# Kernel optimization log

Hardware: AMD Instinct MI355X
Metric: run time of the kernel (lower is better)

## Reference

```python
import jax, jax.numpy as jnp
import numpy as np

N_CODES = 8192
CODE_DIM = 256


def setup_inputs() -> dict:
    key = jax.random.key(0)
    kx, ke = jax.random.split(key)
    x = jax.random.normal(kx, (16, 4096, CODE_DIM), dtype=jnp.float32)
    # nn.Embedding weight initialized uniform(-1/n, 1/n)
    emb = jax.random.uniform(ke, (N_CODES, CODE_DIM), dtype=jnp.float32,
                             minval=-1.0 / N_CODES, maxval=1.0 / N_CODES)
    return {"x": x, "emb": emb}


def reference(x, emb):
    B, T, D = x.shape
    flat = x.reshape(-1, D)                                   # [BT, D]
    # squared euclidean distance: ||f||^2 - 2 f.e^T + ||e||^2  -> [BT, N]
    dist = ((flat * flat).sum(axis=1, keepdims=True)
            - 2.0 * flat @ emb.T
            + (emb * emb).sum(axis=1))
    idx = jnp.argmin(dist, axis=1)                            # [BT] int
    quant = emb[idx].reshape(x.shape)                         # [B, T, D]
    # commitment-style loss: mse(stop_grad(quant), x)
    loss = jnp.mean(jnp.square(jax.lax.stop_gradient(quant) - x))
    # straight-through estimator
    y = x + jax.lax.stop_gradient(quant - x)
    return y, idx.reshape(B, T), loss
```

## Files before the change

kernel.cpp:

```cpp
#include <hip/hip_runtime.h>
#include <stdint.h>


#define NCODES 8192
#define DDIM   256
#define BT     65536

#define TM     128
#define TN     128
#define NSEG   256
#define F4S    17

#define CAPC   48
#define MARGIN 7e-4f
#define TOKPB  128
#define CCODES 64
#define CHUNKS 128
#define KSCALE 1048576.0f
#define KOFF   131072.0f
#define KMARG  737
#define FTOK   32

typedef float  f32x4  __attribute__((ext_vector_type(4)));
typedef __bf16 bf16x8 __attribute__((ext_vector_type(8)));

#define GLDS16(g, l) __builtin_amdgcn_global_load_lds(                         \
    (const __attribute__((address_space(1))) void*)(g),                        \
    (__attribute__((address_space(3))) void*)(l), 16, 0, 0)
#define GLDS4(g, l) __builtin_amdgcn_global_load_lds(                          \
    (const __attribute__((address_space(1))) void*)(g),                        \
    (__attribute__((address_space(3))) void*)(l), 4, 0, 0)

__device__ __forceinline__ unsigned int fenc(float f) {
  unsigned int u = __float_as_uint(f);
  return (u & 0x80000000u) ? ~u : (u | 0x80000000u);
}
__device__ __forceinline__ float fdec(unsigned int u) {
  unsigned int v = (u & 0x80000000u) ? (u ^ 0x80000000u) : ~u;
  return __uint_as_float(v);
}

__device__ __forceinline__ float np_pairwise256_sq(const float4* __restrict__ row) {
#pragma clang fp contract(off)
  float half[2];
  #pragma unroll
  for (int h = 0; h < 2; h++) {
    float r0,r1,r2,r3,r4,r5,r6,r7;
    float4 q0 = row[h*32 + 0];
    float4 q1 = row[h*32 + 1];
    r0 = q0.x*q0.x; r1 = q0.y*q0.y; r2 = q0.z*q0.z; r3 = q0.w*q0.w;
    r4 = q1.x*q1.x; r5 = q1.y*q1.y; r6 = q1.z*q1.z; r7 = q1.w*q1.w;
    #pragma unroll
    for (int g = 1; g < 16; g++) {
      q0 = row[h*32 + g*2];
      q1 = row[h*32 + g*2 + 1];
      r0 += q0.x*q0.x; r1 += q0.y*q0.y; r2 += q0.z*q0.z; r3 += q0.w*q0.w;
      r4 += q1.x*q1.x; r5 += q1.y*q1.y; r6 += q1.z*q1.z; r7 += q1.w*q1.w;
    }
    half[h] = ((r0+r1) + (r2+r3)) + ((r4+r5) + (r6+r7));
  }
  return half[0] + half[1];
}

__device__ __forceinline__ float exact_score_g(const float4* __restrict__ xr,
                                               const float4* __restrict__ er,
                                               float Ar, float Cv) {
#pragma clang fp contract(off)
  float b = 0.0f;
  #pragma unroll 8
  for (int q = 0; q < 64; ++q) {
    const float4 xv = xr[q];
    const float4 ev = er[q];
    b = fmaf(xv.x, ev.x, b);
    b = fmaf(xv.y, ev.y, b);
    b = fmaf(xv.z, ev.z, b);
    b = fmaf(xv.w, ev.w, b);
  }
  const float t1 = fmaf(-2.0f, b, Ar);
  return t1 + Cv;
}

__device__ __forceinline__ void exact_score2_g(const float4* __restrict__ xr,
                                               const float4* __restrict__ e1,
                                               const float4* __restrict__ e2,
                                               float Ar, float Cv1, float Cv2,
                                               float& s1, float& s2) {
#pragma clang fp contract(off)
  float b1 = 0.0f, b2 = 0.0f;
  #pragma unroll 8
  for (int q = 0; q < 64; ++q) {
    const float4 xv = xr[q];
    const float4 v1 = e1[q], v2 = e2[q];
    b1 = fmaf(xv.x, v1.x, b1); b2 = fmaf(xv.x, v2.x, b2);
    b1 = fmaf(xv.y, v1.y, b1); b2 = fmaf(xv.y, v2.y, b2);
    b1 = fmaf(xv.z, v1.z, b1); b2 = fmaf(xv.z, v2.z, b2);
    b1 = fmaf(xv.w, v1.w, b1); b2 = fmaf(xv.w, v2.w, b2);
  }
  s1 = fmaf(-2.0f, b1, Ar) + Cv1;
  s2 = fmaf(-2.0f, b2, Ar) + Cv2;
}

__global__ void vq_pre_a(const float* __restrict__ x, float* __restrict__ Astage) {
  const int t = blockIdx.x * 256 + threadIdx.x;
  Astage[t] = np_pairwise256_sq((const float4*)(x + (size_t)t * DDIM));
}

__global__ void vq_pre_c(const float* __restrict__ emb, float* __restrict__ Cws) {
  const int c = blockIdx.x * 256 + threadIdx.x;
  Cws[c] = np_pairwise256_sq((const float4*)(emb + (size_t)c * DDIM));
}

__global__ void vq_init(float* __restrict__ oloss) { *oloss = 0.0f; }

__global__ void vq_pre_e(const float* __restrict__ emb, uint4* __restrict__ ebf) {
  const int g   = blockIdx.x * 256 + threadIdx.x;
  const int c   = g >> 5;
  const int blk = g & 31;
  const float4* e4 = (const float4*)(emb + (size_t)c * DDIM);
  float4 f0 = e4[blk*2], f1 = e4[blk*2 + 1];
  union { unsigned short us[8]; uint4 v; } pk;
  pk.us[0] = __builtin_bit_cast(unsigned short, (__bf16)f0.x);
  pk.us[1] = __builtin_bit_cast(unsigned short, (__bf16)f0.y);
  pk.us[2] = __builtin_bit_cast(unsigned short, (__bf16)f0.z);
  pk.us[3] = __builtin_bit_cast(unsigned short, (__bf16)f0.w);
  pk.us[4] = __builtin_bit_cast(unsigned short, (__bf16)f1.x);
  pk.us[5] = __builtin_bit_cast(unsigned short, (__bf16)f1.y);
  pk.us[6] = __builtin_bit_cast(unsigned short, (__bf16)f1.z);
  pk.us[7] = __builtin_bit_cast(unsigned short, (__bf16)f1.w);
  ebf[(size_t)c * 32 + (blk ^ (c & 7))] = pk.v;
}

__device__ __forceinline__ void stage_chunk(const char* __restrict__ ebf,
                                            const float* __restrict__ Cws,
                                            int ch, char* ebuf_dst,
                                            float* cs_dst, int tid) {
  const char* src = ebf + (size_t)ch * 32768 + (size_t)tid * 16;
  char* dst = ebuf_dst + (size_t)tid * 16;
  #pragma unroll
  for (int i = 0; i < 4; ++i) GLDS16(src + i * 8192, dst + i * 8192);
  if (tid < 64)
    GLDS4((const char*)Cws + (size_t)ch * 256 + (size_t)tid * 4,
          (char*)cs_dst + (size_t)tid * 4);
}

__global__ __launch_bounds__(512, 4)
void vq_filter(const float* __restrict__ x, const char* __restrict__ ebf,
               const float* __restrict__ Cws, int* __restrict__ cntG,
               int* __restrict__ candG) {
  __shared__ __align__(16) char ebuf[2][32768];
  __shared__ float Cs[2][64];
  __shared__ unsigned int umin[TOKPB];
  __shared__ int cntL[TOKPB];

  const int tid  = threadIdx.x;
  const int lane = tid & 63;
  const int wid  = tid >> 6;
  const int wm   = wid >> 2;
  const int wn   = wid & 3;
  const int l15  = lane & 15;
  const int lhi  = lane >> 4;
  const int tok0 = blockIdx.x * TOKPB;

  if (tid < TOKPB) { umin[tid] = 0xFFFFFFFFu; cntL[tid] = 0; }

  stage_chunk(ebf, Cws, 0, ebuf[0], Cs[0], tid);

  const float4* x4 = (const float4*)x;
  bf16x8 xb[2][8];
  #pragma unroll
  for (int n = 0; n < 2; ++n) {
    const size_t trow = (size_t)(tok0 + wn * 32 + n * 16 + l15) * 64;
    #pragma unroll
    for (int kk = 0; kk < 8; ++kk) {
      float4 f0 = x4[trow + kk * 8 + lhi * 2];
      float4 f1 = x4[trow + kk * 8 + lhi * 2 + 1];
      bf16x8 v;
      v[0] = (__bf16)f0.x; v[1] = (__bf16)f0.y; v[2] = (__bf16)f0.z; v[3] = (__bf16)f0.w;
      v[4] = (__bf16)f1.x; v[5] = (__bf16)f1.y; v[6] = (__bf16)f1.z; v[7] = (__bf16)f1.w;
      xb[n][kk] = v;
    }
  }
  __syncthreads();

  const f32x4 zf = {0.f, 0.f, 0.f, 0.f};
  float rmin[2] = {1e30f, 1e30f};

  for (int c = 0; c < CHUNKS; ++c) {
    stage_chunk(ebf, Cws, (c + 1) & (CHUNKS - 1), ebuf[(c + 1) & 1],
                Cs[(c + 1) & 1], tid);

    const char* ecur = ebuf[c & 1];
    f32x4 acc[2][2];
    #pragma unroll
    for (int kk = 0; kk < 8; ++kk) {
      bf16x8 a[2];
      #pragma unroll
      for (int m = 0; m < 2; ++m) {
        const int row = wm * 32 + m * 16 + l15;
        const int blk = (kk * 4 + lhi) ^ (row & 7);
        a[m] = *(const bf16x8*)(ecur + row * 512 + blk * 16);
      }
      #pragma unroll
      for (int m = 0; m < 2; ++m)
        #pragma unroll
        for (int n = 0; n < 2; ++n)
          acc[m][n] = __builtin_amdgcn_mfma_f32_16x16x32_bf16(
              a[m], xb[n][kk], (kk == 0) ? zf : acc[m][n], 0, 0, 0);
    }

    const float* Csc = Cs[c & 1];
    float cvals[2][4];
    #pragma unroll
    for (int m = 0; m < 2; ++m)
      #pragma unroll
      for (int r = 0; r < 4; ++r)
        cvals[m][r] = Csc[wm * 32 + m * 16 + lhi * 4 + r];

    #pragma unroll
    for (int n = 0; n < 2; ++n) {
      const int t = wn * 32 + n * 16 + l15;
      float s[8];
      float mn = 1e30f;
      #pragma unroll
      for (int m = 0; m < 2; ++m)
        #pragma unroll
        for (int r = 0; r < 4; ++r) {
          const float v = fmaf(-2.0f, acc[m][n][r], cvals[m][r]);
          s[m * 4 + r] = v;
          mn = fminf(mn, v);
        }
      mn = fminf(mn, __shfl_xor(mn, 16));
      mn = fminf(mn, __shfl_xor(mn, 32));
      if (mn < rmin[n]) {
        rmin[n] = mn;
        if (lhi == 0) atomicMin(&umin[t], fenc(mn));
      }
      const float thr = fminf(rmin[n], fdec(umin[t])) + MARGIN;
      #pragma unroll
      for (int m = 0; m < 2; ++m)
        #pragma unroll
        for (int r = 0; r < 4; ++r) {
          if (s[m * 4 + r] <= thr) {
            const int code = c * CCODES + wm * 32 + m * 16 + lhi * 4 + r;
            int key = (int)fmaf(s[m * 4 + r], KSCALE, KOFF);
            key = min(max(key, 0), 262143);
            const int pos = atomicAdd(&cntL[t], 1);
            if (pos < CAPC)
              candG[(size_t)(tok0 + t) * CAPC + pos] = (key << 13) | code;
          }
        }
    }

    __syncthreads();
  }

  {
    const int t4  = tid >> 2;
    const int j4  = tid & 3;
    const int cnt = cntL[t4];
    const int gt4 = tok0 + t4;
    int mask = 0, nk = 0;
    int ent[12];
    if (cnt <= CAPC) {
      const int keyF = min(max((int)fmaf(fdec(umin[t4]), KSCALE, KOFF), 0), 262143);
      const int thrk = keyF + KMARG;
      #pragma unroll
      for (int jj = 0; jj < 12; ++jj) {
        const int j = j4 + jj * 4;
        int e = 0;
        if (j < cnt) {
          e = candG[(size_t)gt4 * CAPC + j];
          if ((e >> 13) <= thrk) { mask |= 1 << jj; ++nk; }
        }
        ent[jj] = e;
      }
    }
    const int b1 = __shfl_up(nk, 1, 4);
    const int b2 = __shfl_up(nk, 2, 4);
    const int b3 = __shfl_up(nk, 3, 4);
    const int base = ((j4 >= 1) ? b1 : 0) + ((j4 >= 2) ? b2 : 0)
                   + ((j4 >= 3) ? b3 : 0);
    int tot = nk;
    tot += __shfl_xor(tot, 1, 4);
    tot += __shfl_xor(tot, 2, 4);
    __syncthreads();
    if (cnt <= CAPC) {
      #pragma unroll
      for (int jj = 0; jj < 12; ++jj)
        if ((mask >> jj) & 1)
          candG[(size_t)gt4 * CAPC + base +
                __builtin_popcount(mask & ((1u << jj) - 1))] = ent[jj];
      if (j4 == 0) cntG[gt4] = tot;
    } else if (j4 == 0) {
      cntG[gt4] = cnt;
    }
  }
}

__global__ __launch_bounds__(256, 8)
void vq_finalize(const float* __restrict__ x, const float* __restrict__ emb,
                 const float* __restrict__ Cws, const int* __restrict__ cntG,
                 const int* __restrict__ candG, float* __restrict__ y,
                 float* __restrict__ oidx, float* __restrict__ oloss,
                 float* __restrict__ lossP) {
  __shared__ int   idx_sh[FTOK];
  __shared__ int   ovf_list[FTOK];
  __shared__ int   n_ovf;
  __shared__ float rbv[256];
  __shared__ int   rbi[256];
  __shared__ float red[4];

  const int tid  = threadIdx.x;
  const int tok0 = blockIdx.x * FTOK;
  const float4* x4g = (const float4*)x;
  const float4* e4g = (const float4*)emb;

  if (tid == 0) n_ovf = 0;
  __syncthreads();

  const int t  = tid >> 3;
  const int j0 = tid & 7;
  const int gt = tok0 + t;
  const int cnt = cntG[gt];
  const float4* xr = x4g + (size_t)gt * 64;

  if (cnt <= CAPC) {
    if (cnt <= 1) {
      if (j0 == 0) {
        const int c = candG[(size_t)gt * CAPC] & 8191;
        idx_sh[t] = c; oidx[gt] = (float)(c + 1);
      }
    } else {
      const float Ar = np_pairwise256_sq(xr);
      float best = 1e30f; int bid = 0x7FFFFFFF;
      for (int j = j0; j < cnt; j += 8) {
        const int c = candG[(size_t)gt * CAPC + j] & 8191;
        const float s = exact_score_g(xr, e4g + (size_t)c * 64, Ar, Cws[c]);
        if (s < best || (s == best && c < bid)) { best = s; bid = c; }
      }
      #pragma unroll
      for (int off = 1; off <= 4; off <<= 1) {
        const float ob = __shfl_xor(best, off);
        const int   oi = __shfl_xor(bid, off);
        if (ob < best || (ob == best && oi < bid)) { best = ob; bid = oi; }
      }
      if (j0 == 0) { idx_sh[t] = bid; oidx[gt] = (float)(bid + 1); }
    }
  } else if (j0 == 0) {
    ovf_list[atomicAdd(&n_ovf, 1)] = t;
  }
  __syncthreads();

  for (int o = 0; o < n_ovf; ++o) {
    const int tt = ovf_list[o];
    const float4* xrr = x4g + (size_t)(tok0 + tt) * 64;
    const float At = np_pairwise256_sq(xrr);
    float bv = 1e30f; int bi2 = 0x7FFFFFFF;
    for (int c0 = tid; c0 < NCODES; c0 += 512) {
      const int c1 = c0 + 256;
      float s1, s2;
      exact_score2_g(xrr, e4g + (size_t)c0 * 64, e4g + (size_t)c1 * 64,
                     At, Cws[c0], Cws[c1], s1, s2);
      if (s1 < bv || (s1 == bv && c0 < bi2)) { bv = s1; bi2 = c0; }
      if (s2 < bv || (s2 == bv && c1 < bi2)) { bv = s2; bi2 = c1; }
    }
    rbv[tid] = bv; rbi[tid] = bi2;
    __syncthreads();
    #pragma unroll
    for (int sft = 128; sft; sft >>= 1) {
      if (tid < sft) {
        const float v2 = rbv[tid + sft]; const int i2 = rbi[tid + sft];
        if (v2 < rbv[tid] || (v2 == rbv[tid] && i2 < rbi[tid])) {
          rbv[tid] = v2; rbi[tid] = i2;
        }
      }
      __syncthreads();
    }
    if (tid == 0) { idx_sh[tt] = rbi[0]; oidx[tok0 + tt] = (float)(rbi[0] + 1); }
    __syncthreads();
  }
  __syncthreads();

  float lsum = 0.0f;
  float4* y4 = (float4*)y;
  #pragma unroll
  for (int r = 0; r < 8; ++r) {
    const int g = tid + 256 * r, row = g >> 6, c4 = g & 63;
    const float4 ev = e4g[(size_t)idx_sh[row] * 64 + c4];
    const float4 xv = x4g[(size_t)(tok0 + row) * 64 + c4];
    y4[(size_t)(tok0 + row) * 64 + c4] = ev;
    const float dx = ev.x - xv.x, dy = ev.y - xv.y, dz = ev.z - xv.z, dw = ev.w - xv.w;
    lsum += dx * dx + dy * dy + dz * dz + dw * dw;
  }
  #pragma unroll
  for (int off = 32; off; off >>= 1) lsum += __shfl_down(lsum, off);
  if ((tid & 63) == 0) red[tid >> 6] = lsum;
  __syncthreads();
  if (tid == 0) {
    const float s = red[0] + red[1] + red[2] + red[3];
    if (lossP) lossP[blockIdx.x] = s;
    else       atomicAdd(oloss, s);
  }
}

__global__ void vq_fin(float* __restrict__ oloss,
                       const float* __restrict__ lossP, int n) {
  __shared__ float sh[4];
  if (n > 0) {
    float s = 0.0f;
    for (int i = threadIdx.x; i < n; i += 256) s += lossP[i];
    #pragma unroll
    for (int off = 32; off; off >>= 1) s += __shfl_down(s, off);
    if ((threadIdx.x & 63) == 0) sh[threadIdx.x >> 6] = s;
    __syncthreads();
    if (threadIdx.x == 0)
      *oloss = (sh[0] + sh[1] + sh[2] + sh[3]) * (1.0f / 16777216.0f);
  } else {
    if (threadIdx.x == 0) *oloss = *oloss * (1.0f / 16777216.0f);
  }
}

__global__ __launch_bounds__(256, 2)
void vq_main(const float* __restrict__ x, const float* __restrict__ emb,
             const float* __restrict__ Cws, float* __restrict__ y,
             float* __restrict__ oidx, float* __restrict__ oloss) {
  __shared__ float4 xs4[TM * F4S];
  __shared__ float4 es4[TN * F4S];
  __shared__ float  Cs[TN];
  __shared__ int    idx_sh[TM];
  __shared__ float  red[4];

  const int tid = threadIdx.x;
  const int ry = tid >> 4;
  const int rx = tid & 15;
  const int tok0 = blockIdx.x * TM;

  const float4* x4g = (const float4*)x;
  const float4* e4g = (const float4*)emb;

  float A_reg[8];
  #pragma unroll
  for (int m = 0; m < 8; m++) A_reg[m] = oidx[tok0 + ry + 16 * m];

  float best[8];
  int   i1[8];
  #pragma unroll
  for (int m = 0; m < 8; m++) { best[m] = 1e30f; i1[m] = 0; }

  float acc[8][8];

  for (int seg = 0; seg < NSEG; ++seg) {
    const int chunk = seg >> 2;
    const int kq = seg & 3;
    __syncthreads();
    #pragma unroll
    for (int h = 0; h < 2; h++) {
      float4 t[4];
      #pragma unroll
      for (int q = 0; q < 4; q++) {
        const int r = h * 4 + q;
        t[q] = x4g[(size_t)(tok0 + ry + 16 * r) * 64 + kq * 16 + rx];
      }
      #pragma unroll
      for (int q = 0; q < 4; q++) {
        const int r = h * 4 + q;
        xs4[(ry + 16 * r) * F4S + rx] = t[q];
      }
    }
    #pragma unroll
    for (int h = 0; h < 2; h++) {
      float4 t[4];
      #pragma unroll
      for (int q = 0; q < 4; q++) {
        const int r = h * 4 + q;
        t[q] = e4g[(size_t)(chunk * TN + ry + 16 * r) * 64 + kq * 16 + rx];
      }
      #pragma unroll
      for (int q = 0; q < 4; q++) {
        const int r = h * 4 + q;
        es4[(ry + 16 * r) * F4S + rx] = t[q];
      }
    }
    if (kq == 0 && tid < TN) Cs[tid] = Cws[chunk * TN + tid];
    __syncthreads();

    if (kq == 0) {
      #pragma unroll
      for (int m = 0; m < 8; m++)
        #pragma unroll
        for (int n = 0; n < 8; n++) acc[m][n] = 0.0f;
    }

    #pragma unroll
    for (int k4 = 0; k4 < 16; k4++) {
      float4 a[8], b[8];
      #pragma unroll
      for (int m = 0; m < 8; m++) a[m] = xs4[(ry + 16 * m) * F4S + k4];
      #pragma unroll
      for (int n = 0; n < 8; n++) b[n] = es4[(rx + 16 * n) * F4S + k4];
      #pragma unroll
      for (int m = 0; m < 8; m++)
        #pragma unroll
        for (int n = 0; n < 8; n++) {
          acc[m][n] = fmaf(a[m].x, b[n].x, acc[m][n]);
          acc[m][n] = fmaf(a[m].y, b[n].y, acc[m][n]);
          acc[m][n] = fmaf(a[m].z, b[n].z, acc[m][n]);
          acc[m][n] = fmaf(a[m].w, b[n].w, acc[m][n]);
        }
    }

    if (kq == 3) {
      const int c0 = chunk * TN;
      #pragma unroll
      for (int n = 0; n < 8; n++) {
        const float Cv = Cs[rx + 16 * n];
        const int c = c0 + rx + 16 * n;
        #pragma unroll
        for (int m = 0; m < 8; m++) {
          const float t1 = fmaf(-2.0f, acc[m][n], A_reg[m]);
          const float t2 = t1 + Cv;
          if (t2 < best[m]) { best[m] = t2; i1[m] = c; }
        }
      }
    }
  }

  __syncthreads();
  float* bv1 = (float*)xs4;
  int*   bi  = (int*)es4;
  #pragma unroll
  for (int m = 0; m < 8; m++) {
    bv1[(ry + 16 * m) * 16 + rx] = best[m];
    bi [(ry + 16 * m) * 16 + rx] = i1[m];
  }
  __syncthreads();
  if (tid < TM) {
    float v = bv1[tid * 16];
    int   id = bi[tid * 16];
    for (int t = 1; t < 16; t++) {
      const float vv = bv1[tid * 16 + t];
      const int   ii = bi [tid * 16 + t];
      if (vv < v || (vv == v && ii < id)) { v = vv; id = ii; }
    }
    idx_sh[tid] = id;
    oidx[tok0 + tid] = (float)(id + 1);
  }
  __syncthreads();

  float lsum = 0.0f;
  float4* y4 = (float4*)y;
  #pragma unroll
  for (int r = 0; r < 32; r++) {
    const int g = tid + 256 * r, row = g >> 6, c4 = g & 63;
    const float4 ev = e4g[(size_t)idx_sh[row] * 64 + c4];
    const float4 xv = x4g[(size_t)(tok0 + row) * 64 + c4];
    y4[(size_t)(tok0 + row) * 64 + c4] = ev;
    const float dx = ev.x - xv.x, dy = ev.y - xv.y, dz = ev.z - xv.z, dw = ev.w - xv.w;
    lsum += dx * dx + dy * dy + dz * dz + dw * dw;
  }
  #pragma unroll
  for (int off = 32; off; off >>= 1) lsum += __shfl_down(lsum, off);
  if ((tid & 63) == 0) red[tid >> 6] = lsum;
  __syncthreads();
  if (tid == 0) atomicAdd(oloss, red[0] + red[1] + red[2] + red[3]);
}

extern "C" void kernel_launch(void* const* d_in, const int* in_sizes, int n_in,
                              void* d_out, int out_size, void* d_ws, size_t ws_size,
                              hipStream_t stream) {
  const float* x   = (const float*)d_in[0];
  const float* emb = (const float*)d_in[1];

  float* y     = (float*)d_out;
  float* oidx  = y + (size_t)BT * DDIM;
  float* oloss = oidx + BT;

  char*  wsB   = (char*)d_ws;
  float* Cws   = (float*)wsB;
  int*   cntG  = (int*)(wsB + 32768);
  char*  ebf   = wsB + 32768 + 262144;
  int*   candG = (int*)(wsB + 294912 + 4194304);
  float* lossP = (float*)(wsB + 294912 + 4194304 + (size_t)BT * CAPC * 4);
  const size_t NEED  = 294912 + 4194304 + (size_t)BT * CAPC * 4;
  const size_t NEED2 = NEED + (size_t)(BT / FTOK) * 4;

  vq_init <<<1, 1,           0, stream>>>(oloss);
  vq_pre_c<<<NCODES/256,256, 0, stream>>>(emb, Cws);

  if (ws_size >= NEED) {
    float* lp = (ws_size >= NEED2) ? lossP : nullptr;
    vq_pre_e   <<<1024, 256, 0, stream>>>(emb, (uint4*)ebf);
    vq_filter  <<<BT/TOKPB, 512, 0, stream>>>(x, ebf, Cws, cntG, candG);
    vq_finalize<<<BT/FTOK, 256, 0, stream>>>(x, emb, Cws, cntG, candG,
                                             y, oidx, oloss, lp);
    vq_fin     <<<1, 256, 0, stream>>>(oloss, lp, lp ? (BT / FTOK) : 0);
  } else {
    vq_pre_a<<<BT / 256, 256, 0, stream>>>(x, oidx);
    vq_main <<<BT / TM, 256,  0, stream>>>(x, emb, Cws, y, oidx, oloss);
    vq_fin  <<<1, 256, 0, stream>>>(oloss, nullptr, 0);
  }
}
```

Measured before the change: 760.3 us.

## Split finalize into select, global overflow queue, and gather kernels

The fused finalize kernel becomes three kernels. A per-token select kernel does the candidate rescoring with one thread per token and pushes overflow tokens onto a global queue. A grid-strided overflow kernel brute-forces the queued tokens across many blocks, and a gather kernel writes y and the per-block loss partials. The intent is to stop a few overflow tokens from serializing whole finalize blocks. The cost is extra launches, a global atomic, and a select loop run by one thread per token instead of eight, plus reuse of the bf16 codebook workspace for the queue after the filter has run.

Measured after the change: 853.2 us. 1.12x slower.

```diff
diff --git a/kernel.cpp b/kernel.cpp
--- a/kernel.cpp
+++ b/kernel.cpp
@@ -19,7 +19,7 @@
 #define KSCALE 1048576.0f
 #define KOFF   131072.0f
 #define KMARG  737
-#define FTOK   32
+#define GBLK   32
 
 typedef float  f32x4  __attribute__((ext_vector_type(4)));
 typedef __bf16 bf16x8 __attribute__((ext_vector_type(8)));
@@ -111,6 +111,8 @@
 }
 
 __global__ void vq_init(float* __restrict__ oloss) { *oloss = 0.0f; }
+
+__global__ void vq_zq(int* __restrict__ qcnt) { *qcnt = 0; }
 
 __global__ void vq_pre_e(const float* __restrict__ emb, uint4* __restrict__ ebf) {
   const int g   = blockIdx.x * 256 + threadIdx.x;
@@ -298,68 +300,51 @@
 }
 
 __global__ __launch_bounds__(256, 8)
-void vq_finalize(const float* __restrict__ x, const float* __restrict__ emb,
-                 const float* __restrict__ Cws, const int* __restrict__ cntG,
-                 const int* __restrict__ candG, float* __restrict__ y,
-                 float* __restrict__ oidx, float* __restrict__ oloss,
-                 float* __restrict__ lossP) {
-  __shared__ int   idx_sh[FTOK];
-  __shared__ int   ovf_list[FTOK];
-  __shared__ int   n_ovf;
+void vq_select(const float* __restrict__ x, const float* __restrict__ emb,
+               const float* __restrict__ Cws, const int* __restrict__ cntG,
+               const int* __restrict__ candG, float* __restrict__ oidx,
+               int* __restrict__ queue, int* __restrict__ qcnt) {
+  const int gt = blockIdx.x * 256 + threadIdx.x;
+  const int cnt = cntG[gt];
+  if (cnt > CAPC) {
+    queue[atomicAdd(qcnt, 1)] = gt;
+    return;
+  }
+  const int e0 = candG[(size_t)gt * CAPC] & 8191;
+  if (cnt <= 1) {
+    oidx[gt] = (float)(e0 + 1);
+    return;
+  }
+  const float4* xr = (const float4*)x + (size_t)gt * 64;
+  const float4* e4g = (const float4*)emb;
+  const float Ar = np_pairwise256_sq(xr);
+  float best = 1e30f; int bid = 0x7FFFFFFF;
+  for (int j = 0; j < cnt; ++j) {
+    const int c = candG[(size_t)gt * CAPC + j] & 8191;
+    const float s = exact_score_g(xr, e4g + (size_t)c * 64, Ar, Cws[c]);
+    if (s < best || (s == best && c < bid)) { best = s; bid = c; }
+  }
+  oidx[gt] = (float)(bid + 1);
+}
+
+__global__ __launch_bounds__(256, 4)
+void vq_ovf(const float* __restrict__ x, const float* __restrict__ emb,
+            const float* __restrict__ Cws, const int* __restrict__ queue,
+            const int* __restrict__ qcnt, float* __restrict__ oidx) {
   __shared__ float rbv[256];
   __shared__ int   rbi[256];
-  __shared__ float red[4];
-
-  const int tid  = threadIdx.x;
-  const int tok0 = blockIdx.x * FTOK;
-  const float4* x4g = (const float4*)x;
+  const int tid = threadIdx.x;
   const float4* e4g = (const float4*)emb;
-
-  if (tid == 0) n_ovf = 0;
-  __syncthreads();
-
-  const int t  = tid >> 3;
-  const int j0 = tid & 7;
-  const int gt = tok0 + t;
-  const int cnt = cntG[gt];
-  const float4* xr = x4g + (size_t)gt * 64;
-
-  if (cnt <= CAPC) {
-    if (cnt <= 1) {
-      if (j0 == 0) {
-        const int c = candG[(size_t)gt * CAPC] & 8191;
-        idx_sh[t] = c; oidx[gt] = (float)(c + 1);
-      }
-    } else {
-      const float Ar = np_pairwise256_sq(xr);
-      float best = 1e30f; int bid = 0x7FFFFFFF;
-      for (int j = j0; j < cnt; j += 8) {
-        const int c = candG[(size_t)gt * CAPC + j] & 8191;
-        const float s = exact_score_g(xr, e4g + (size_t)c * 64, Ar, Cws[c]);
-        if (s < best || (s == best && c < bid)) { best = s; bid = c; }
-      }
-      #pragma unroll
-      for (int off = 1; off <= 4; off <<= 1) {
-        const float ob = __shfl_xor(best, off);
-        const int   oi = __shfl_xor(bid, off);
-        if (ob < best || (ob == best && oi < bid)) { best = ob; bid = oi; }
-      }
-      if (j0 == 0) { idx_sh[t] = bid; oidx[gt] = (float)(bid + 1); }
-    }
-  } else if (j0 == 0) {
-    ovf_list[atomicAdd(&n_ovf, 1)] = t;
-  }
-  __syncthreads();
-
-  for (int o = 0; o < n_ovf; ++o) {
-    const int tt = ovf_list[o];
-    const float4* xrr = x4g + (size_t)(tok0 + tt) * 64;
-    const float At = np_pairwise256_sq(xrr);
+  const int nq = *qcnt;
+  for (int i = blockIdx.x; i < nq; i += gridDim.x) {
+    const int gt = queue[i];
+    const float4* xr = (const float4*)x + (size_t)gt * 64;
+    const float At = np_pairwise256_sq(xr);
     float bv = 1e30f; int bi2 = 0x7FFFFFFF;
     for (int c0 = tid; c0 < NCODES; c0 += 512) {
       const int c1 = c0 + 256;
       float s1, s2;
-      exact_score2_g(xrr, e4g + (size_t)c0 * 64, e4g + (size_t)c1 * 64,
+      exact_score2_g(xr, e4g + (size_t)c0 * 64, e4g + (size_t)c1 * 64,
                      At, Cws[c0], Cws[c1], s1, s2);
       if (s1 < bv || (s1 == bv && c0 < bi2)) { bv = s1; bi2 = c0; }
       if (s2 < bv || (s2 == bv && c1 < bi2)) { bv = s2; bi2 = c1; }
@@ -376,9 +361,23 @@
       }
       __syncthreads();
     }
-    if (tid == 0) { idx_sh[tt] = rbi[0]; oidx[tok0 + tt] = (float)(rbi[0] + 1); }
+    if (tid == 0) oidx[gt] = (float)(rbi[0] + 1);
     __syncthreads();
   }
+}
+
+__global__ __launch_bounds__(256, 8)
+void vq_gather(const float* __restrict__ x, const float* __restrict__ emb,
+               const float* __restrict__ oidx, float* __restrict__ y,
+               float* __restrict__ lossP) {
+  __shared__ int   idx_sh[GBLK];
+  __shared__ float red[4];
+  const int tid  = threadIdx.x;
+  const int tok0 = blockIdx.x * GBLK;
+  const float4* x4g = (const float4*)x;
+  const float4* e4g = (const float4*)emb;
+
+  if (tid < GBLK) idx_sh[tid] = (int)oidx[tok0 + tid] - 1;
   __syncthreads();
 
   float lsum = 0.0f;
@@ -396,11 +395,7 @@
   for (int off = 32; off; off >>= 1) lsum += __shfl_down(lsum, off);
   if ((tid & 63) == 0) red[tid >> 6] = lsum;
   __syncthreads();
-  if (tid == 0) {
-    const float s = red[0] + red[1] + red[2] + red[3];
-    if (lossP) lossP[blockIdx.x] = s;
-    else       atomicAdd(oloss, s);
-  }
+  if (tid == 0) lossP[blockIdx.x] = red[0] + red[1] + red[2] + red[3];
 }
 
 __global__ void vq_fin(float* __restrict__ oloss,
@@ -580,20 +575,23 @@
   int*   cntG  = (int*)(wsB + 32768);
   char*  ebf   = wsB + 32768 + 262144;
   int*   candG = (int*)(wsB + 294912 + 4194304);
-  float* lossP = (float*)(wsB + 294912 + 4194304 + (size_t)BT * CAPC * 4);
-  const size_t NEED  = 294912 + 4194304 + (size_t)BT * CAPC * 4;
-  const size_t NEED2 = NEED + (size_t)(BT / FTOK) * 4;
+  int*   queue = (int*)ebf;
+  int*   qcnt  = (int*)(ebf + 262144);
+  float* lossP = (float*)(ebf + 262400);
+  const size_t NEED = 294912 + 4194304 + (size_t)BT * CAPC * 4;
 
   vq_init <<<1, 1,           0, stream>>>(oloss);
   vq_pre_c<<<NCODES/256,256, 0, stream>>>(emb, Cws);
 
   if (ws_size >= NEED) {
-    float* lp = (ws_size >= NEED2) ? lossP : nullptr;
-    vq_pre_e   <<<1024, 256, 0, stream>>>(emb, (uint4*)ebf);
-    vq_filter  <<<BT/TOKPB, 512, 0, stream>>>(x, ebf, Cws, cntG, candG);
-    vq_finalize<<<BT/FTOK, 256, 0, stream>>>(x, emb, Cws, cntG, candG,
-                                             y, oidx, oloss, lp);
-    vq_fin     <<<1, 256, 0, stream>>>(oloss, lp, lp ? (BT / FTOK) : 0);
+    vq_pre_e <<<1024, 256, 0, stream>>>(emb, (uint4*)ebf);
+    vq_filter<<<BT/TOKPB, 512, 0, stream>>>(x, ebf, Cws, cntG, candG);
+    vq_zq    <<<1, 1, 0, stream>>>(qcnt);
+    vq_select<<<BT/256, 256, 0, stream>>>(x, emb, Cws, cntG, candG,
+                                          oidx, queue, qcnt);
+    vq_ovf   <<<512, 256, 0, stream>>>(x, emb, Cws, queue, qcnt, oidx);
+    vq_gather<<<BT/GBLK, 256, 0, stream>>>(x, emb, oidx, y, lossP);
+    vq_fin   <<<1, 256, 0, stream>>>(oloss, lossP, BT / GBLK);
   } else {
     vq_pre_a<<<BT / 256, 256, 0, stream>>>(x, oidx);
     vq_main <<<BT / TM, 256,  0, stream>>>(x, emb, Cws, y, oidx, oloss);
```
